# Optimization experiments

Hardware: AMD Instinct MI355X
Metric: run time of the kernel (lower is better)

Reference implementation:

```python
import jax, jax.numpy as jnp
import numpy as np

N, E, B = 100000, 800000, 64
IN, HC1, HC2, NC, SA = 256, 128, 32, 2, 350
NEG = 0.2  # GATv2Conv default negative_slope


def forward(s_x, s_edge_index, s_batch, s_root_n_id,
            Wq, bq, Wk, bk, Wv, bv,
            Wl1, bl1, Wr1, br1, att1, bias1,
            Wl2, bl2, Wr2, br2, att2, bias2,
            Wl3, bl3, Wr3, br3, att3, bias3,
            c1w, c1b, c2W, c2b, c3W, c3b,
            linW, linb, aW1, ab1, aW2, mW1, mb1, mW2, mb2):
    src, dst = s_edge_index[0], s_edge_index[1]
    x_info = s_x
    # --- SelfAttention over seq_len=1 (x.unsqueeze(1)) ---
    z = s_x[:, None, :]                                   # [N,1,IN]
    q = z @ Wq + bq; k = z @ Wk + bk; v = z @ Wv + bv      # [N,1,SA]
    scores = jnp.einsum('nqd,nkd->nqk', q, k) / jnp.sqrt(jnp.float32(SA))
    probs = jax.nn.softmax(scores, axis=-1)
    h = jnp.einsum('nqk,nkd->nqd', probs, v)[:, 0, :]      # [N,SA]

    def gatv2(x, Wl, bl, Wr, br, att, bias):
        # PyG GATv2Conv, heads=1, eval mode (dropout off)
        xl = x @ Wl + bl                                   # source transform [N,O]
        xr = x @ Wr + br                                   # target transform [N,O]
        e = jax.nn.leaky_relu(xl[src] + xr[dst], NEG)      # [E,O]
        s = e @ att                                        # [E]
        smax = jax.ops.segment_max(s, dst, num_segments=N)
        smax = jnp.where(jnp.isfinite(smax), smax, 0.0)
        ex = jnp.exp(s - smax[dst])
        den = jax.ops.segment_sum(ex, dst, num_segments=N)
        alpha = ex / jnp.maximum(den[dst], 1e-16)
        return jax.ops.segment_sum(alpha[:, None] * xl[src], dst, num_segments=N) + bias

    h = jax.nn.relu(gatv2(h, Wl1, bl1, Wr1, br1, att1, bias1))
    h = jax.nn.relu(gatv2(h, Wl2, bl2, Wr2, br2, att2, bias2))
    h = jax.nn.relu(gatv2(h, Wl3, bl3, Wr3, br3, att3, bias3))   # [N,HC2]

    # --- readout: root node feature ++ global mean pool ---
    cnt = jax.ops.segment_sum(jnp.ones((N,), h.dtype), s_batch, num_segments=B)
    pooled = jax.ops.segment_sum(h, s_batch, num_segments=B) / jnp.maximum(cnt, 1.0)[:, None]
    sx = jnp.concatenate([h[s_root_n_id], pooled], axis=-1)       # [B,2*HC2]

    # --- info branch on raw root features ---
    info = x_info[s_root_n_id]                                    # [B,IN]
    info = c1w[0] * info[:, :-2] + c1w[1] * info[:, 1:-1] + c1w[2] * info[:, 2:] + c1b  # Conv1d(1,1,3)
    t = info.T                                                    # [IN-2,B]
    t = jax.nn.relu(c2W @ t + c2b[:, None])                       # [HC1,B]
    t = jax.nn.relu(c3W @ t + c3b[:, None])                       # [HC1//2,B]
    t = t.T                                                       # [B,HC1//2]
    L = t.shape[1]
    t = jax.nn.relu(t.reshape(B, HC2, L // HC2).mean(-1))         # AdaptiveAvgPool1d(HC2)

    sx = jax.nn.relu(sx @ linW + linb)                            # [B,HC2]

    # --- semantic attention over the two views ---
    emb = jnp.stack([sx, t], axis=1)                              # [B,2,HC2]
    w = jnp.tanh(emb @ aW1 + ab1) @ aW2                           # [B,2,1]
    beta = jax.nn.softmax(w, axis=1)
    emb = (beta * emb).sum(1)                                     # [B,HC2]

    return jax.nn.softmax(jnp.tanh(emb @ mW1 + mb1) @ mW2 + mb2, axis=1)  # [B,NC]


def setup_inputs() -> dict:
    keys = iter(jax.random.split(jax.random.key(0), 64))
    def nrm(*shape):
        return jax.random.normal(next(keys), shape, dtype=jnp.float32) * 0.05
    inp = {}
    inp['s_x'] = jax.random.normal(next(keys), (N, IN), dtype=jnp.float32)
    inp['s_edge_index'] = jax.random.randint(next(keys), (2, E), 0, N)
    inp['s_batch'] = jnp.sort(jax.random.randint(next(keys), (N,), 0, B))
    inp['s_root_n_id'] = jax.random.randint(next(keys), (B,), 0, N)
    inp['Wq'] = nrm(IN, SA); inp['bq'] = nrm(SA)
    inp['Wk'] = nrm(IN, SA); inp['bk'] = nrm(SA)
    inp['Wv'] = nrm(IN, SA); inp['bv'] = nrm(SA)
    inp['Wl1'] = nrm(SA, HC1); inp['bl1'] = nrm(HC1)
    inp['Wr1'] = nrm(SA, HC1); inp['br1'] = nrm(HC1)
    inp['att1'] = nrm(HC1); inp['bias1'] = nrm(HC1)
    inp['Wl2'] = nrm(HC1, HC1 // 2); inp['bl2'] = nrm(HC1 // 2)
    inp['Wr2'] = nrm(HC1, HC1 // 2); inp['br2'] = nrm(HC1 // 2)
    inp['att2'] = nrm(HC1 // 2); inp['bias2'] = nrm(HC1 // 2)
    inp['Wl3'] = nrm(HC1 // 2, HC2); inp['bl3'] = nrm(HC2)
    inp['Wr3'] = nrm(HC1 // 2, HC2); inp['br3'] = nrm(HC2)
    inp['att3'] = nrm(HC2); inp['bias3'] = nrm(HC2)
    inp['c1w'] = nrm(3); inp['c1b'] = nrm(1)
    inp['c2W'] = nrm(HC1, IN - 2); inp['c2b'] = nrm(HC1)
    inp['c3W'] = nrm(HC1 // 2, HC1); inp['c3b'] = nrm(HC1 // 2)
    inp['linW'] = nrm(2 * HC2, HC2); inp['linb'] = nrm(HC2)
    inp['aW1'] = nrm(HC2, 16); inp['ab1'] = nrm(16); inp['aW2'] = nrm(16, 1)
    inp['mW1'] = nrm(HC2, 16); inp['mb1'] = nrm(16)
    inp['mW2'] = nrm(16, NC); inp['mb2'] = nrm(NC)
    return inp


def reference(s_x, s_edge_index, s_batch, s_root_n_id,
              Wq, bq, Wk, bk, Wv, bv,
              Wl1, bl1, Wr1, br1, att1, bias1,
              Wl2, bl2, Wr2, br2, att2, bias2,
              Wl3, bl3, Wr3, br3, att3, bias3,
              c1w, c1b, c2W, c2b, c3W, c3b,
              linW, linb, aW1, ab1, aW2, mW1, mb1, mW2, mb2):
    return forward(s_x, s_edge_index, s_batch, s_root_n_id,
                   Wq, bq, Wk, bk, Wv, bv,
                   Wl1, bl1, Wr1, br1, att1, bias1,
                   Wl2, bl2, Wr2, br2, att2, bias2,
                   Wl3, bl3, Wr3, br3, att3, bias3,
                   c1w, c1b, c2W, c2b, c3W, c3b,
                   linW, linb, aW1, ab1, aW2, mW1, mb1, mW2, mb2)
```

## Files before the change

kernel.cpp:

```cpp
#include <hip/hip_runtime.h>
#include <hip/hip_bf16.h>
#include <math.h>

typedef unsigned short ushort_t;
typedef __attribute__((ext_vector_type(8))) short bfrag;
typedef __attribute__((ext_vector_type(4))) float ffrag;

constexpr int N_NODES = 100000;
constexpr int N_EDGES = 800000;
constexpr int NB      = 64;
constexpr int IN_F    = 256;
constexpr int HC1C    = 128;
constexpr int HC2C    = 32;
constexpr int SA_D    = 350;
constexpr float NEG   = 0.2f;

constexpr int SCAN_NBLK = (N_NODES + 255) / 256;
constexpr int MB128     = (N_NODES + 127) / 128;

constexpr size_t OFF_WT1    = 0;
constexpr size_t OFF_WT2    = OFF_WT1 + 65536;
constexpr size_t OFF_WT3    = OFF_WT2 + 16384;
constexpr size_t OFF_BC1    = OFF_WT3 + 4096;
constexpr size_t OFF_BC2    = OFF_BC1 + 256;
constexpr size_t OFF_BC3    = OFF_BC2 + 128;
constexpr size_t OFF_XLR    = OFF_BC3 + 64;
constexpr size_t OFF_H      = OFF_XLR + (size_t)N_NODES * 256;
constexpr size_t OFF_DEG    = OFF_H + (size_t)N_NODES * 128;
constexpr size_t OFF_ROWPTR = OFF_DEG + N_NODES;
constexpr size_t OFF_CURSOR = OFF_ROWPTR + N_NODES + 1;
constexpr size_t OFF_BLKS   = OFF_CURSOR + N_NODES;
constexpr size_t OFF_BLKO   = OFF_BLKS + 512;
constexpr size_t OFF_CSRSRC = OFF_BLKO + 512;
constexpr size_t OFF_POOLED = OFF_CSRSRC + N_EDGES;
constexpr size_t OFF_CNT    = OFF_POOLED + NB * HC2C;
constexpr size_t OFF_SX     = OFF_CNT + NB;
constexpr size_t OFF_INFO   = OFF_SX + NB * HC2C;
constexpr size_t OFF_T1     = OFF_INFO + (size_t)NB * (IN_F - 2);
constexpr size_t OFF_T2     = OFF_T1 + (size_t)HC1C * NB;
constexpr size_t OFF_TT     = OFF_T2 + (size_t)NB * NB;
constexpr size_t WS_FLOATS  = OFF_TT + NB * HC2C;

__device__ __forceinline__ ushort_t f2bf(float f) {
  union { float f; unsigned int u; } a;
  a.f = f;
  unsigned int r = a.u + 0x7FFFu + ((a.u >> 16) & 1u);
  return (ushort_t)(r >> 16);
}
__device__ __forceinline__ float bf2f(ushort_t h) {
  union { unsigned int u; float f; } a;
  a.u = ((unsigned int)h) << 16;
  return a.f;
}
__device__ __forceinline__ float2 bfp(unsigned int u) {
  float2 r;
  r.x = __uint_as_float(u << 16);
  r.y = __uint_as_float(u & 0xFFFF0000u);
  return r;
}
__device__ __forceinline__ unsigned int pack2(float a, float b) {
  unsigned int ua = __float_as_uint(a);
  ua += 0x7FFFu + ((ua >> 16) & 1u);
  unsigned int ub = __float_as_uint(b);
  ub += 0x7FFFu + ((ub >> 16) & 1u);
  return __builtin_amdgcn_perm(ub, ua, 0x07060302u);
}

__global__ void k_wcomb(const float* __restrict__ Wv, const float* __restrict__ Wl1,
                        const float* __restrict__ Wr1, ushort_t* __restrict__ WT) {
  int t = blockIdx.x * blockDim.x + threadIdx.x;
  if (t >= 256 * 256) return;
  int n = t & 255;
  int k = t >> 8;
  const float* Wx = (n < 128) ? Wl1 : Wr1;
  int j = n & 127;
  float a = 0.f;
  for (int kk = 0; kk < SA_D; ++kk) a += Wv[k * SA_D + kk] * Wx[kk * 128 + j];
  WT[(size_t)n * 256 + k] = f2bf(a);
}

__global__ void k_bcomb(const float* __restrict__ bv, const float* __restrict__ Wl1,
                        const float* __restrict__ bl1, const float* __restrict__ Wr1,
                        const float* __restrict__ br1, float* __restrict__ bc) {
  int n = threadIdx.x;
  if (n >= 256) return;
  const float* Wx = (n < 128) ? Wl1 : Wr1;
  const float* bx = (n < 128) ? bl1 : br1;
  int j = n & 127;
  float a = bx[j];
  for (int kk = 0; kk < SA_D; ++kk) a += bv[kk] * Wx[kk * 128 + j];
  bc[n] = a;
}

template <int K, int C>
__global__ void k_wpack(const float* __restrict__ Wl, const float* __restrict__ bl,
                        const float* __restrict__ Wr, const float* __restrict__ br,
                        ushort_t* __restrict__ WT, float* __restrict__ bc) {
  constexpr int NN = 2 * C;
  int t = blockIdx.x * blockDim.x + threadIdx.x;
  if (t < NN) bc[t] = (t < C) ? bl[t] : br[t - C];
  if (t >= NN * K) return;
  int n = t % NN;
  int k = t / NN;
  float v = (n < C) ? Wl[k * C + n] : Wr[k * C + (n - C)];
  WT[(size_t)n * K + k] = f2bf(v);
}

__global__ void k_hist(const int* __restrict__ dst, int* __restrict__ deg) {
  int e = blockIdx.x * blockDim.x + threadIdx.x;
  if (e < N_EDGES) atomicAdd(deg + dst[e], 1);
}

__global__ void k_scan_local(const int* __restrict__ deg, int* __restrict__ row_ptr,
                             int* __restrict__ blk_sum) {
  __shared__ int sh[256];
  int t = threadIdx.x;
  int i = blockIdx.x * 256 + t;
  int v = (i < N_NODES) ? deg[i] : 0;
  sh[t] = v;
  __syncthreads();
  for (int off = 1; off < 256; off <<= 1) {
    int add = (t >= off) ? sh[t - off] : 0;
    __syncthreads();
    sh[t] += add;
    __syncthreads();
  }
  if (i < N_NODES) row_ptr[i] = sh[t] - v;
  if (t == 255) blk_sum[blockIdx.x] = sh[255];
}

__global__ void k_scan_blk(const int* __restrict__ blk_sum, int* __restrict__ blk_off) {
  __shared__ int sh[512];
  int t = threadIdx.x;
  int v = (t < SCAN_NBLK) ? blk_sum[t] : 0;
  sh[t] = v;
  __syncthreads();
  for (int off = 1; off < 512; off <<= 1) {
    int add = (t >= off) ? sh[t - off] : 0;
    __syncthreads();
    sh[t] += add;
    __syncthreads();
  }
  blk_off[t] = sh[t] - v;
}

__global__ void k_scan_add(int* __restrict__ row_ptr, const int* __restrict__ blk_off,
                           int* __restrict__ cursor) {
  int i = blockIdx.x * blockDim.x + threadIdx.x;
  if (i < N_NODES) {
    int v = row_ptr[i] + blk_off[i >> 8];
    row_ptr[i] = v;
    cursor[i] = v;
  }
  if (i == 0) row_ptr[N_NODES] = N_EDGES;
}

__global__ void k_fill(const int* __restrict__ src, const int* __restrict__ dst,
                       int* __restrict__ cursor, int* __restrict__ csr_src) {
  int e = blockIdx.x * blockDim.x + threadIdx.x;
  if (e >= N_EDGES) return;
  int pos = atomicAdd(cursor + dst[e], 1);
  csr_src[pos] = src[e];
}

template <int K, int NN, int BN, bool AF32>
__global__ __launch_bounds__(256) void k_gemm_bf16(const void* __restrict__ xin,
                                                   const ushort_t* __restrict__ WT,
                                                   const float* __restrict__ bc,
                                                   ushort_t* __restrict__ out, int M) {
  constexpr int BM    = 128;
  constexpr int BK    = 64;
  constexpr int LDA   = BK + 8;
  constexpr int RT    = 4;
  constexpr int CT    = BN / 32;
  constexpr int NSTEP = K / BK;
  __shared__ ushort_t As[BM * LDA];
  __shared__ ushort_t Bs[BN * LDA];
  const int tid  = threadIdx.x;
  const int wave = tid >> 6;
  const int wrow = wave >> 1;
  const int wcol = wave & 1;
  const int lane = tid & 63;
  const int quad = lane >> 4;
  const int l16  = lane & 15;
  const int m0   = blockIdx.x * BM;
  const int n0   = blockIdx.y * BN;

  const int arow = tid >> 1;
  const int aks  = (tid & 1) * 32;
  int gm = m0 + arow;
  if (gm >= M) gm = M - 1;

  ffrag acc[RT][CT];
#pragma unroll
  for (int rt = 0; rt < RT; ++rt)
#pragma unroll
    for (int ct = 0; ct < CT; ++ct) acc[rt][ct] = ffrag{0.f, 0.f, 0.f, 0.f};

  for (int i = 0; i < NSTEP; ++i) {
    const int k0 = i * BK;
    if (i) __syncthreads();
    if (AF32) {
      const float4* sp = (const float4*)((const float*)xin + (size_t)gm * K + k0 + aks);
      float4 f[8];
#pragma unroll
      for (int j = 0; j < 8; ++j) f[j] = sp[j];
      unsigned int d[16];
#pragma unroll
      for (int j = 0; j < 8; ++j) {
        d[2 * j]     = pack2(f[j].x, f[j].y);
        d[2 * j + 1] = pack2(f[j].z, f[j].w);
      }
#pragma unroll
      for (int j = 0; j < 4; ++j)
        *(uint4*)&As[arow * LDA + aks + j * 8] = *(uint4*)&d[j * 4];
    } else {
      const uint4* sp = (const uint4*)((const ushort_t*)xin + (size_t)gm * K + k0 + aks);
      uint4 u[4];
#pragma unroll
      for (int j = 0; j < 4; ++j) u[j] = sp[j];
#pragma unroll
      for (int j = 0; j < 4; ++j)
        *(uint4*)&As[arow * LDA + aks + j * 8] = u[j];
    }
#pragma unroll
    for (int c = 0; c < BN / 32; ++c) {
      int ch = tid + c * 256;
      int n  = ch >> 3;
      int ks = (ch & 7) * 8;
      *(uint4*)&Bs[n * LDA + ks] = *(const uint4*)(WT + (size_t)(n0 + n) * K + k0 + ks);
    }
    __syncthreads();
#pragma unroll
    for (int kh = 0; kh < 2; ++kh) {
      bfrag a[RT], b[CT];
#pragma unroll
      for (int rt = 0; rt < RT; ++rt)
        a[rt] = *(const bfrag*)&As[(wrow * 64 + rt * 16 + l16) * LDA + kh * 32 + quad * 8];
#pragma unroll
      for (int ct = 0; ct < CT; ++ct)
        b[ct] = *(const bfrag*)&Bs[(wcol * (BN / 2) + ct * 16 + l16) * LDA + kh * 32 + quad * 8];
#pragma unroll
      for (int ct = 0; ct < CT; ++ct)
#pragma unroll
        for (int rt = 0; rt < RT; ++rt)
          acc[rt][ct] = __builtin_amdgcn_mfma_f32_16x16x32_bf16(a[rt], b[ct], acc[rt][ct], 0, 0, 0);
    }
  }

#pragma unroll
  for (int rt = 0; rt < RT; ++rt)
#pragma unroll
    for (int ct = 0; ct < CT; ++ct) {
      int n = n0 + wcol * (BN / 2) + ct * 16 + l16;
      float b = bc[n];
#pragma unroll
      for (int r = 0; r < 4; ++r) {
        int m = m0 + wrow * 64 + rt * 16 + quad * 4 + r;
        if (m < M) out[(size_t)m * NN + n] = f2bf(acc[rt][ct][r] + b);
      }
    }
}

template <int C>
__global__ void k_gat(const ushort_t* __restrict__ xlr, const int* __restrict__ row_ptr,
                      const int* __restrict__ csr_src, const float* __restrict__ att,
                      const float* __restrict__ bias, ushort_t* __restrict__ h) {
  constexpr int G = C / 8;
  constexpr int RS = 2 * C;
  int t = blockIdx.x * blockDim.x + threadIdx.x;
  int d = t / G;
  int lane = t - d * G;
  if (d >= N_NODES) return;
  float xr[8], a[8];
  {
    uint4 u = *(const uint4*)(xlr + (size_t)d * RS + C + lane * 8);
    float2 p0 = bfp(u.x), p1 = bfp(u.y), p2 = bfp(u.z), p3 = bfp(u.w);
    xr[0] = p0.x; xr[1] = p0.y; xr[2] = p1.x; xr[3] = p1.y;
    xr[4] = p2.x; xr[5] = p2.y; xr[6] = p3.x; xr[7] = p3.y;
  }
  *(float4*)&a[0] = *(const float4*)(att + lane * 8);
  *(float4*)&a[4] = *(const float4*)(att + lane * 8 + 4);
  float acc[8];
#pragma unroll
  for (int j = 0; j < 8; ++j) acc[j] = 0.f;
  float den = 0.f;
  const int e0 = row_ptr[d], e1 = row_ptr[d + 1];
  int i = e0;
  for (; i + 2 <= e1; i += 2) {
    int s0 = csr_src[i];
    int s1 = csr_src[i + 1];
    uint4 u0 = *(const uint4*)(xlr + (size_t)s0 * RS + lane * 8);
    uint4 u1 = *(const uint4*)(xlr + (size_t)s1 * RS + lane * 8);
    float xl0[8], xl1[8];
    {
      float2 q0 = bfp(u0.x), q1 = bfp(u0.y), q2 = bfp(u0.z), q3 = bfp(u0.w);
      xl0[0] = q0.x; xl0[1] = q0.y; xl0[2] = q1.x; xl0[3] = q1.y;
      xl0[4] = q2.x; xl0[5] = q2.y; xl0[6] = q3.x; xl0[7] = q3.y;
      float2 r0 = bfp(u1.x), r1 = bfp(u1.y), r2 = bfp(u1.z), r3 = bfp(u1.w);
      xl1[0] = r0.x; xl1[1] = r0.y; xl1[2] = r1.x; xl1[3] = r1.y;
      xl1[4] = r2.x; xl1[5] = r2.y; xl1[6] = r3.x; xl1[7] = r3.y;
    }
    float p0 = 0.f, p1 = 0.f;
#pragma unroll
    for (int j = 0; j < 8; ++j) {
      float v0 = xl0[j] + xr[j];
      v0 = v0 > 0.f ? v0 : NEG * v0;
      p0 += a[j] * v0;
      float v1 = xl1[j] + xr[j];
      v1 = v1 > 0.f ? v1 : NEG * v1;
      p1 += a[j] * v1;
    }
#pragma unroll
    for (int off = G / 2; off > 0; off >>= 1) {
      p0 += __shfl_xor(p0, off, 64);
      p1 += __shfl_xor(p1, off, 64);
    }
    float ex0 = expf(p0);
    float ex1 = expf(p1);
    den += ex0 + ex1;
#pragma unroll
    for (int j = 0; j < 8; ++j) acc[j] += ex0 * xl0[j] + ex1 * xl1[j];
  }
  if (i < e1) {
    int s = csr_src[i];
    uint4 u = *(const uint4*)(xlr + (size_t)s * RS + lane * 8);
    float xl[8];
    {
      float2 q0 = bfp(u.x), q1 = bfp(u.y), q2 = bfp(u.z), q3 = bfp(u.w);
      xl[0] = q0.x; xl[1] = q0.y; xl[2] = q1.x; xl[3] = q1.y;
      xl[4] = q2.x; xl[5] = q2.y; xl[6] = q3.x; xl[7] = q3.y;
    }
    float p = 0.f;
#pragma unroll
    for (int j = 0; j < 8; ++j) {
      float v = xl[j] + xr[j];
      v = v > 0.f ? v : NEG * v;
      p += a[j] * v;
    }
#pragma unroll
    for (int off = G / 2; off > 0; off >>= 1) p += __shfl_xor(p, off, 64);
    float ex = expf(p);
    den += ex;
#pragma unroll
    for (int j = 0; j < 8; ++j) acc[j] += ex * xl[j];
  }
  float inv = 1.f / fmaxf(den, 1e-16f);
  float o[8];
#pragma unroll
  for (int j = 0; j < 8; ++j)
    o[j] = fmaxf(acc[j] * inv + bias[lane * 8 + j], 0.f);
  uint4 pk;
  pk.x = pack2(o[0], o[1]);
  pk.y = pack2(o[2], o[3]);
  pk.z = pack2(o[4], o[5]);
  pk.w = pack2(o[6], o[7]);
  *(uint4*)(h + (size_t)d * C + lane * 8) = pk;
}

__global__ void k_pool(const ushort_t* __restrict__ h3, const int* __restrict__ batch,
                       float* __restrict__ pooled, float* __restrict__ cnt) {
  constexpr int NPB = 1024;
  constexpr int NPT = NPB / 8;
  int c = threadIdx.x & 31;
  int r = threadIdx.x >> 5;
  int base = blockIdx.x * NPB + r * NPT;
  if (base >= N_NODES) return;
  int end = base + NPT;
  if (end > N_NODES) end = N_NODES;
  int cur_b = batch[base];
  float acc = 0.f, count = 0.f;
  for (int n = base; n < end; ++n) {
    int b = batch[n];
    if (b != cur_b) {
      atomicAdd(pooled + cur_b * HC2C + c, acc);
      if (c == 0) atomicAdd(cnt + cur_b, count);
      cur_b = b;
      acc = 0.f;
      count = 0.f;
    }
    acc += bf2f(h3[(size_t)n * HC2C + c]);
    count += 1.f;
  }
  atomicAdd(pooled + cur_b * HC2C + c, acc);
  if (c == 0) atomicAdd(cnt + cur_b, count);
}

__global__ void k_sx(const ushort_t* __restrict__ h3, const int* __restrict__ root,
                     const float* __restrict__ pooled, const float* __restrict__ cnt,
                     const float* __restrict__ linW, const float* __restrict__ linb,
                     float* __restrict__ sx) {
  int t = blockIdx.x * blockDim.x + threadIdx.x;
  if (t >= NB * HC2C) return;
  int b = t >> 5, j = t & 31;
  int r = root[b];
  float inv = 1.f / fmaxf(cnt[b], 1.0f);
  float a = linb[j];
  for (int c = 0; c < HC2C; ++c) a += bf2f(h3[(size_t)r * HC2C + c]) * linW[c * HC2C + j];
  for (int c = 0; c < HC2C; ++c) a += (pooled[b * HC2C + c] * inv) * linW[(HC2C + c) * HC2C + j];
  sx[t] = a > 0.f ? a : 0.f;
}

__global__ void k_info1(const float* __restrict__ X, const int* __restrict__ root,
                        const float* __restrict__ c1w, const float* __restrict__ c1b,
                        float* __restrict__ info) {
  constexpr int L = IN_F - 2;
  int t = blockIdx.x * blockDim.x + threadIdx.x;
  if (t >= NB * L) return;
  int b = t / L, i = t - (t / L) * L;
  const float* xr = X + (size_t)root[b] * IN_F;
  info[t] = c1w[0] * xr[i] + c1w[1] * xr[i + 1] + c1w[2] * xr[i + 2] + c1b[0];
}

__global__ void k_info2(const float* __restrict__ info, const float* __restrict__ c2W,
                        const float* __restrict__ c2b, float* __restrict__ t1) {
  constexpr int L = IN_F - 2;
  int t = blockIdx.x * blockDim.x + threadIdx.x;
  if (t >= HC1C * NB) return;
  int j = t >> 6, b = t & 63;
  float a = c2b[j];
  for (int i = 0; i < L; ++i) a += c2W[j * L + i] * info[b * L + i];
  t1[t] = a > 0.f ? a : 0.f;
}

__global__ void k_info3(const float* __restrict__ t1, const float* __restrict__ c3W,
                        const float* __restrict__ c3b, float* __restrict__ t2) {
  int t = blockIdx.x * blockDim.x + threadIdx.x;
  if (t >= NB * NB) return;
  int j = t >> 6, b = t & 63;
  float a = c3b[j];
  for (int i = 0; i < HC1C; ++i) a += c3W[j * HC1C + i] * t1[i * NB + b];
  t2[t] = a > 0.f ? a : 0.f;
}

__global__ void k_info4(const float* __restrict__ t2, float* __restrict__ tt) {
  int t = blockIdx.x * blockDim.x + threadIdx.x;
  if (t >= NB * HC2C) return;
  int b = t >> 5, c = t & 31;
  float v = 0.5f * (t2[(2 * c) * NB + b] + t2[(2 * c + 1) * NB + b]);
  tt[b * HC2C + c] = v > 0.f ? v : 0.f;
}

__global__ void k_final(const float* __restrict__ sx, const float* __restrict__ tt,
                        const float* __restrict__ aW1, const float* __restrict__ ab1,
                        const float* __restrict__ aW2, const float* __restrict__ mW1,
                        const float* __restrict__ mb1, const float* __restrict__ mW2,
                        const float* __restrict__ mb2, float* __restrict__ out) {
  int b = threadIdx.x;
  if (b >= NB) return;
  const float* e0 = sx + b * HC2C;
  const float* e1 = tt + b * HC2C;
  float w[2];
#pragma unroll
  for (int r = 0; r < 2; ++r) {
    const float* eb = (r == 0) ? e0 : e1;
    float acc = 0.f;
    for (int j = 0; j < 16; ++j) {
      float z = ab1[j];
      for (int c = 0; c < HC2C; ++c) z += eb[c] * aW1[c * 16 + j];
      acc += tanhf(z) * aW2[j];
    }
    w[r] = acc;
  }
  float mx = fmaxf(w[0], w[1]);
  float x0 = expf(w[0] - mx), x1 = expf(w[1] - mx);
  float inv = 1.f / (x0 + x1);
  float b0 = x0 * inv, b1 = x1 * inv;
  float t16[16];
  for (int j = 0; j < 16; ++j) {
    float z = mb1[j];
    for (int c = 0; c < HC2C; ++c) z += (b0 * e0[c] + b1 * e1[c]) * mW1[c * 16 + j];
    t16[j] = tanhf(z);
  }
  float l0 = mb2[0], l1 = mb2[1];
  for (int j = 0; j < 16; ++j) {
    l0 += t16[j] * mW2[j * 2 + 0];
    l1 += t16[j] * mW2[j * 2 + 1];
  }
  float m2 = fmaxf(l0, l1);
  float y0 = expf(l0 - m2), y1 = expf(l1 - m2);
  float is = 1.f / (y0 + y1);
  out[b * 2 + 0] = y0 * is;
  out[b * 2 + 1] = y1 * is;
}

extern "C" void kernel_launch(void* const* d_in, const int* in_sizes, int n_in, void* d_out,
                              int out_size, void* d_ws, size_t ws_size, hipStream_t stream) {
  if (ws_size < WS_FLOATS * sizeof(float)) return;

  const float* s_x   = (const float*)d_in[0];
  const int*   edge  = (const int*)d_in[1];
  const int*   batch = (const int*)d_in[2];
  const int*   root  = (const int*)d_in[3];
  const float* Wv    = (const float*)d_in[8];
  const float* bv    = (const float*)d_in[9];
  const float* Wl1   = (const float*)d_in[10];
  const float* bl1   = (const float*)d_in[11];
  const float* Wr1   = (const float*)d_in[12];
  const float* br1   = (const float*)d_in[13];
  const float* att1  = (const float*)d_in[14];
  const float* bias1 = (const float*)d_in[15];
  const float* Wl2   = (const float*)d_in[16];
  const float* bl2   = (const float*)d_in[17];
  const float* Wr2   = (const float*)d_in[18];
  const float* br2   = (const float*)d_in[19];
  const float* att2  = (const float*)d_in[20];
  const float* bias2 = (const float*)d_in[21];
  const float* Wl3   = (const float*)d_in[22];
  const float* bl3   = (const float*)d_in[23];
  const float* Wr3   = (const float*)d_in[24];
  const float* br3   = (const float*)d_in[25];
  const float* att3  = (const float*)d_in[26];
  const float* bias3 = (const float*)d_in[27];
  const float* c1w   = (const float*)d_in[28];
  const float* c1b   = (const float*)d_in[29];
  const float* c2W   = (const float*)d_in[30];
  const float* c2b   = (const float*)d_in[31];
  const float* c3W   = (const float*)d_in[32];
  const float* c3b   = (const float*)d_in[33];
  const float* linW  = (const float*)d_in[34];
  const float* linb  = (const float*)d_in[35];
  const float* aW1   = (const float*)d_in[36];
  const float* ab1   = (const float*)d_in[37];
  const float* aW2   = (const float*)d_in[38];
  const float* mW1   = (const float*)d_in[39];
  const float* mb1   = (const float*)d_in[40];
  const float* mW2   = (const float*)d_in[41];
  const float* mb2   = (const float*)d_in[42];

  const int* src = edge;
  const int* dst = edge + N_EDGES;

  float*    ws      = (float*)d_ws;
  ushort_t* WT1     = (ushort_t*)(ws + OFF_WT1);
  ushort_t* WT2     = (ushort_t*)(ws + OFF_WT2);
  ushort_t* WT3     = (ushort_t*)(ws + OFF_WT3);
  float*    bc1     = ws + OFF_BC1;
  float*    bc2     = ws + OFF_BC2;
  float*    bc3     = ws + OFF_BC3;
  ushort_t* xlr     = (ushort_t*)(ws + OFF_XLR);
  ushort_t* hbuf    = (ushort_t*)(ws + OFF_H);
  int*      deg     = (int*)(ws + OFF_DEG);
  int*      row_ptr = (int*)(ws + OFF_ROWPTR);
  int*      cursor  = (int*)(ws + OFF_CURSOR);
  int*      blks    = (int*)(ws + OFF_BLKS);
  int*      blko    = (int*)(ws + OFF_BLKO);
  int*      csr_src = (int*)(ws + OFF_CSRSRC);
  float*    pooled  = ws + OFF_POOLED;
  float*    cnt     = ws + OFF_CNT;
  float*    sx      = ws + OFF_SX;
  float*    info    = ws + OFF_INFO;
  float*    t1      = ws + OFF_T1;
  float*    t2      = ws + OFF_T2;
  float*    tt      = ws + OFF_TT;
  float*    out     = (float*)d_out;

  hipMemsetAsync(deg, 0, N_NODES * sizeof(int), stream);
  k_hist<<<(N_EDGES + 255) / 256, 256, 0, stream>>>(dst, deg);
  k_scan_local<<<SCAN_NBLK, 256, 0, stream>>>(deg, row_ptr, blks);
  k_scan_blk<<<1, 512, 0, stream>>>(blks, blko);
  k_scan_add<<<SCAN_NBLK, 256, 0, stream>>>(row_ptr, blko, cursor);
  k_fill<<<(N_EDGES + 255) / 256, 256, 0, stream>>>(src, dst, cursor, csr_src);

  k_wcomb<<<(256 * 256) / 256, 256, 0, stream>>>(Wv, Wl1, Wr1, WT1);
  k_bcomb<<<1, 256, 0, stream>>>(bv, Wl1, bl1, Wr1, br1, bc1);
  k_wpack<128, 64><<<(128 * 128 + 255) / 256, 256, 0, stream>>>(Wl2, bl2, Wr2, br2, WT2, bc2);
  k_wpack<64, 32><<<(64 * 64 + 255) / 256, 256, 0, stream>>>(Wl3, bl3, Wr3, br3, WT3, bc3);

  k_gemm_bf16<256, 256, 128, true><<<dim3(MB128, 2), 256, 0, stream>>>(s_x, WT1, bc1, xlr,
                                                                       N_NODES);
  k_gat<128><<<(N_NODES * 16 + 255) / 256, 256, 0, stream>>>(xlr, row_ptr, csr_src, att1,
                                                             bias1, hbuf);

  k_gemm_bf16<128, 128, 128, false><<<dim3(MB128, 1), 256, 0, stream>>>(hbuf, WT2, bc2, xlr,
                                                                        N_NODES);
  k_gat<64><<<(N_NODES * 8 + 255) / 256, 256, 0, stream>>>(xlr, row_ptr, csr_src, att2,
                                                           bias2, hbuf);

  k_gemm_bf16<64, 64, 64, false><<<dim3(MB128, 1), 256, 0, stream>>>(hbuf, WT3, bc3, xlr,
                                                                     N_NODES);
  k_gat<32><<<(N_NODES * 4 + 255) / 256, 256, 0, stream>>>(xlr, row_ptr, csr_src, att3,
                                                           bias3, hbuf);

  hipMemsetAsync(pooled, 0, (NB * HC2C + NB) * sizeof(float), stream);
  k_pool<<<(N_NODES + 1023) / 1024, 256, 0, stream>>>(hbuf, batch, pooled, cnt);
  k_sx<<<(NB * HC2C + 255) / 256, 256, 0, stream>>>(hbuf, root, pooled, cnt, linW, linb, sx);

  k_info1<<<(NB * (IN_F - 2) + 255) / 256, 256, 0, stream>>>(s_x, root, c1w, c1b, info);
  k_info2<<<(HC1C * NB + 255) / 256, 256, 0, stream>>>(info, c2W, c2b, t1);
  k_info3<<<(NB * NB + 255) / 256, 256, 0, stream>>>(t1, c3W, c3b, t2);
  k_info4<<<(NB * HC2C + 255) / 256, 256, 0, stream>>>(t2, tt);

  k_final<<<1, NB, 0, stream>>>(sx, tt, aW1, ab1, aW2, mW1, mb1, mW2, mb2, out);
}
```

Measured before the change: 655.1 us.

## Fuse weight-pack and tail kernels, shrink GEMM K-tile, unroll GAT edges by four

Merges the four weight-packing kernels into one launch and the six readout/info/final kernels into one per-graph block kernel that keeps intermediates in shared memory. The bf16 GEMM K-tile drops from 64 to 32, with one MFMA step per tile and a simpler B load. The GAT aggregation loop now handles four edges at a time to put more gathers in flight. The aim is fewer launches and more memory-level parallelism, at the cost of twice as many GEMM barriers and higher register pressure in the GAT loop.

```diff
diff --git a/kernel.cpp b/kernel.cpp
--- a/kernel.cpp
+++ b/kernel.cpp
@@ -34,12 +34,7 @@
 constexpr size_t OFF_CSRSRC = OFF_BLKO + 512;
 constexpr size_t OFF_POOLED = OFF_CSRSRC + N_EDGES;
 constexpr size_t OFF_CNT    = OFF_POOLED + NB * HC2C;
-constexpr size_t OFF_SX     = OFF_CNT + NB;
-constexpr size_t OFF_INFO   = OFF_SX + NB * HC2C;
-constexpr size_t OFF_T1     = OFF_INFO + (size_t)NB * (IN_F - 2);
-constexpr size_t OFF_T2     = OFF_T1 + (size_t)HC1C * NB;
-constexpr size_t OFF_TT     = OFF_T2 + (size_t)NB * NB;
-constexpr size_t WS_FLOATS  = OFF_TT + NB * HC2C;
+constexpr size_t WS_FLOATS  = OFF_CNT + NB;
 
 __device__ __forceinline__ ushort_t f2bf(float f) {
   union { float f; unsigned int u; } a;
@@ -65,45 +60,53 @@
   ub += 0x7FFFu + ((ub >> 16) & 1u);
   return __builtin_amdgcn_perm(ub, ua, 0x07060302u);
 }
-
-__global__ void k_wcomb(const float* __restrict__ Wv, const float* __restrict__ Wl1,
-                        const float* __restrict__ Wr1, ushort_t* __restrict__ WT) {
-  int t = blockIdx.x * blockDim.x + threadIdx.x;
-  if (t >= 256 * 256) return;
-  int n = t & 255;
-  int k = t >> 8;
-  const float* Wx = (n < 128) ? Wl1 : Wr1;
-  int j = n & 127;
-  float a = 0.f;
-  for (int kk = 0; kk < SA_D; ++kk) a += Wv[k * SA_D + kk] * Wx[kk * 128 + j];
-  WT[(size_t)n * 256 + k] = f2bf(a);
-}
-
-__global__ void k_bcomb(const float* __restrict__ bv, const float* __restrict__ Wl1,
-                        const float* __restrict__ bl1, const float* __restrict__ Wr1,
-                        const float* __restrict__ br1, float* __restrict__ bc) {
-  int n = threadIdx.x;
-  if (n >= 256) return;
-  const float* Wx = (n < 128) ? Wl1 : Wr1;
-  const float* bx = (n < 128) ? bl1 : br1;
-  int j = n & 127;
-  float a = bx[j];
-  for (int kk = 0; kk < SA_D; ++kk) a += bv[kk] * Wx[kk * 128 + j];
-  bc[n] = a;
-}
-
-template <int K, int C>
-__global__ void k_wpack(const float* __restrict__ Wl, const float* __restrict__ bl,
-                        const float* __restrict__ Wr, const float* __restrict__ br,
-                        ushort_t* __restrict__ WT, float* __restrict__ bc) {
-  constexpr int NN = 2 * C;
-  int t = blockIdx.x * blockDim.x + threadIdx.x;
-  if (t < NN) bc[t] = (t < C) ? bl[t] : br[t - C];
-  if (t >= NN * K) return;
-  int n = t % NN;
-  int k = t / NN;
-  float v = (n < C) ? Wl[k * C + n] : Wr[k * C + (n - C)];
-  WT[(size_t)n * K + k] = f2bf(v);
+__device__ __forceinline__ void unp8(uint4 u, float* x) {
+  float2 p0 = bfp(u.x), p1 = bfp(u.y), p2 = bfp(u.z), p3 = bfp(u.w);
+  x[0] = p0.x; x[1] = p0.y; x[2] = p1.x; x[3] = p1.y;
+  x[4] = p2.x; x[5] = p2.y; x[6] = p3.x; x[7] = p3.y;
+}
+
+__global__ void k_pack_all(const float* __restrict__ Wv, const float* __restrict__ bv,
+                           const float* __restrict__ Wl1, const float* __restrict__ bl1,
+                           const float* __restrict__ Wr1, const float* __restrict__ br1,
+                           const float* __restrict__ Wl2, const float* __restrict__ bl2,
+                           const float* __restrict__ Wr2, const float* __restrict__ br2,
+                           const float* __restrict__ Wl3, const float* __restrict__ bl3,
+                           const float* __restrict__ Wr3, const float* __restrict__ br3,
+                           ushort_t* __restrict__ WT1, float* __restrict__ bc1,
+                           ushort_t* __restrict__ WT2, float* __restrict__ bc2,
+                           ushort_t* __restrict__ WT3, float* __restrict__ bc3) {
+  int blk = blockIdx.x;
+  int tid = threadIdx.x;
+  if (blk < 256) {
+    int t = blk * 256 + tid;
+    int n = t & 255, k = t >> 8;
+    const float* Wx = (n < 128) ? Wl1 : Wr1;
+    int j = n & 127;
+    float a = 0.f;
+    for (int kk = 0; kk < SA_D; ++kk) a += Wv[k * SA_D + kk] * Wx[kk * 128 + j];
+    WT1[(size_t)n * 256 + k] = f2bf(a);
+  } else if (blk == 256) {
+    int n = tid;
+    const float* Wx = (n < 128) ? Wl1 : Wr1;
+    const float* bx = (n < 128) ? bl1 : br1;
+    int j = n & 127;
+    float a = bx[j];
+    for (int kk = 0; kk < SA_D; ++kk) a += bv[kk] * Wx[kk * 128 + j];
+    bc1[n] = a;
+  } else if (blk < 321) {
+    int t = (blk - 257) * 256 + tid;
+    int n = t & 127, k = t >> 7;
+    if (t < 128) bc2[t] = (t < 64) ? bl2[t] : br2[t - 64];
+    float v = (n < 64) ? Wl2[k * 64 + n] : Wr2[k * 64 + (n - 64)];
+    WT2[(size_t)n * 128 + k] = f2bf(v);
+  } else {
+    int t = (blk - 321) * 256 + tid;
+    int n = t & 63, k = t >> 6;
+    if (t < 64) bc3[t] = (t < 32) ? bl3[t] : br3[t - 32];
+    float v = (n < 32) ? Wl3[k * 32 + n] : Wr3[k * 32 + (n - 32)];
+    WT3[(size_t)n * 64 + k] = f2bf(v);
+  }
 }
 
 __global__ void k_hist(const int* __restrict__ dst, int* __restrict__ deg) {
@@ -169,7 +172,7 @@
                                                    const float* __restrict__ bc,
                                                    ushort_t* __restrict__ out, int M) {
   constexpr int BM    = 128;
-  constexpr int BK    = 64;
+  constexpr int BK    = 32;
   constexpr int LDA   = BK + 8;
   constexpr int RT    = 4;
   constexpr int CT    = BN / 32;
@@ -187,7 +190,7 @@
   const int n0   = blockIdx.y * BN;
 
   const int arow = tid >> 1;
-  const int aks  = (tid & 1) * 32;
+  const int aks  = (tid & 1) * 16;
   int gm = m0 + arow;
   if (gm >= M) gm = M - 1;
 
@@ -202,50 +205,47 @@
     if (i) __syncthreads();
     if (AF32) {
       const float4* sp = (const float4*)((const float*)xin + (size_t)gm * K + k0 + aks);
-      float4 f[8];
-#pragma unroll
-      for (int j = 0; j < 8; ++j) f[j] = sp[j];
-      unsigned int d[16];
-#pragma unroll
-      for (int j = 0; j < 8; ++j) {
+      float4 f[4];
+#pragma unroll
+      for (int j = 0; j < 4; ++j) f[j] = sp[j];
+      unsigned int d[8];
+#pragma unroll
+      for (int j = 0; j < 4; ++j) {
         d[2 * j]     = pack2(f[j].x, f[j].y);
         d[2 * j + 1] = pack2(f[j].z, f[j].w);
       }
-#pragma unroll
-      for (int j = 0; j < 4; ++j)
-        *(uint4*)&As[arow * LDA + aks + j * 8] = *(uint4*)&d[j * 4];
+      *(uint4*)&As[arow * LDA + aks]     = *(uint4*)&d[0];
+      *(uint4*)&As[arow * LDA + aks + 8] = *(uint4*)&d[4];
     } else {
       const uint4* sp = (const uint4*)((const ushort_t*)xin + (size_t)gm * K + k0 + aks);
-      uint4 u[4];
-#pragma unroll
-      for (int j = 0; j < 4; ++j) u[j] = sp[j];
-#pragma unroll
-      for (int j = 0; j < 4; ++j)
-        *(uint4*)&As[arow * LDA + aks + j * 8] = u[j];
-    }
-#pragma unroll
-    for (int c = 0; c < BN / 32; ++c) {
-      int ch = tid + c * 256;
-      int n  = ch >> 3;
-      int ks = (ch & 7) * 8;
-      *(uint4*)&Bs[n * LDA + ks] = *(const uint4*)(WT + (size_t)(n0 + n) * K + k0 + ks);
+      uint4 u0 = sp[0], u1 = sp[1];
+      *(uint4*)&As[arow * LDA + aks]     = u0;
+      *(uint4*)&As[arow * LDA + aks + 8] = u1;
+    }
+    if (BN == 128) {
+      int bn  = tid >> 1;
+      int bks = (tid & 1) * 16;
+      const ushort_t* gp = WT + (size_t)(n0 + bn) * K + k0 + bks;
+      *(uint4*)&Bs[bn * LDA + bks]     = *(const uint4*)gp;
+      *(uint4*)&Bs[bn * LDA + bks + 8] = *(const uint4*)(gp + 8);
+    } else {
+      int bn  = tid >> 2;
+      int bks = (tid & 3) * 8;
+      *(uint4*)&Bs[bn * LDA + bks] = *(const uint4*)(WT + (size_t)(n0 + bn) * K + k0 + bks);
     }
     __syncthreads();
-#pragma unroll
-    for (int kh = 0; kh < 2; ++kh) {
-      bfrag a[RT], b[CT];
+    bfrag a[RT], b[CT];
+#pragma unroll
+    for (int rt = 0; rt < RT; ++rt)
+      a[rt] = *(const bfrag*)&As[(wrow * 64 + rt * 16 + l16) * LDA + quad * 8];
+#pragma unroll
+    for (int ct = 0; ct < CT; ++ct)
+      b[ct] = *(const bfrag*)&Bs[(wcol * (BN / 2) + ct * 16 + l16) * LDA + quad * 8];
+#pragma unroll
+    for (int ct = 0; ct < CT; ++ct)
 #pragma unroll
       for (int rt = 0; rt < RT; ++rt)
-        a[rt] = *(const bfrag*)&As[(wrow * 64 + rt * 16 + l16) * LDA + kh * 32 + quad * 8];
-#pragma unroll
-      for (int ct = 0; ct < CT; ++ct)
-        b[ct] = *(const bfrag*)&Bs[(wcol * (BN / 2) + ct * 16 + l16) * LDA + kh * 32 + quad * 8];
-#pragma unroll
-      for (int ct = 0; ct < CT; ++ct)
-#pragma unroll
-        for (int rt = 0; rt < RT; ++rt)
-          acc[rt][ct] = __builtin_amdgcn_mfma_f32_16x16x32_bf16(a[rt], b[ct], acc[rt][ct], 0, 0, 0);
-    }
+        acc[rt][ct] = __builtin_amdgcn_mfma_f32_16x16x32_bf16(a[rt], b[ct], acc[rt][ct], 0, 0, 0);
   }
 
 #pragma unroll
@@ -273,12 +273,7 @@
   int lane = t - d * G;
   if (d >= N_NODES) return;
   float xr[8], a[8];
-  {
-    uint4 u = *(const uint4*)(xlr + (size_t)d * RS + C + lane * 8);
-    float2 p0 = bfp(u.x), p1 = bfp(u.y), p2 = bfp(u.z), p3 = bfp(u.w);
-    xr[0] = p0.x; xr[1] = p0.y; xr[2] = p1.x; xr[3] = p1.y;
-    xr[4] = p2.x; xr[5] = p2.y; xr[6] = p3.x; xr[7] = p3.y;
-  }
+  unp8(*(const uint4*)(xlr + (size_t)d * RS + C + lane * 8), xr);
   *(float4*)&a[0] = *(const float4*)(att + lane * 8);
   *(float4*)&a[4] = *(const float4*)(att + lane * 8 + 4);
   float acc[8];
@@ -287,50 +282,41 @@
   float den = 0.f;
   const int e0 = row_ptr[d], e1 = row_ptr[d + 1];
   int i = e0;
-  for (; i + 2 <= e1; i += 2) {
-    int s0 = csr_src[i];
-    int s1 = csr_src[i + 1];
-    uint4 u0 = *(const uint4*)(xlr + (size_t)s0 * RS + lane * 8);
-    uint4 u1 = *(const uint4*)(xlr + (size_t)s1 * RS + lane * 8);
-    float xl0[8], xl1[8];
-    {
-      float2 q0 = bfp(u0.x), q1 = bfp(u0.y), q2 = bfp(u0.z), q3 = bfp(u0.w);
-      xl0[0] = q0.x; xl0[1] = q0.y; xl0[2] = q1.x; xl0[3] = q1.y;
-      xl0[4] = q2.x; xl0[5] = q2.y; xl0[6] = q3.x; xl0[7] = q3.y;
-      float2 r0 = bfp(u1.x), r1 = bfp(u1.y), r2 = bfp(u1.z), r3 = bfp(u1.w);
-      xl1[0] = r0.x; xl1[1] = r0.y; xl1[2] = r1.x; xl1[3] = r1.y;
-      xl1[4] = r2.x; xl1[5] = r2.y; xl1[6] = r3.x; xl1[7] = r3.y;
-    }
-    float p0 = 0.f, p1 = 0.f;
+  for (; i + 4 <= e1; i += 4) {
+    uint4 u[4];
+#pragma unroll
+    for (int q = 0; q < 4; ++q)
+      u[q] = *(const uint4*)(xlr + (size_t)csr_src[i + q] * RS + lane * 8);
+    float xl[4][8];
+#pragma unroll
+    for (int q = 0; q < 4; ++q) unp8(u[q], xl[q]);
+    float p[4] = {0.f, 0.f, 0.f, 0.f};
 #pragma unroll
     for (int j = 0; j < 8; ++j) {
-      float v0 = xl0[j] + xr[j];
-      v0 = v0 > 0.f ? v0 : NEG * v0;
-      p0 += a[j] * v0;
-      float v1 = xl1[j] + xr[j];
-      v1 = v1 > 0.f ? v1 : NEG * v1;
-      p1 += a[j] * v1;
+#pragma unroll
+      for (int q = 0; q < 4; ++q) {
+        float v = xl[q][j] + xr[j];
+        v = v > 0.f ? v : NEG * v;
+        p[q] += a[j] * v;
+      }
     }
 #pragma unroll
     for (int off = G / 2; off > 0; off >>= 1) {
-      p0 += __shfl_xor(p0, off, 64);
-      p1 += __shfl_xor(p1, off, 64);
-    }
-    float ex0 = expf(p0);
-    float ex1 = expf(p1);
-    den += ex0 + ex1;
-#pragma unroll
-    for (int j = 0; j < 8; ++j) acc[j] += ex0 * xl0[j] + ex1 * xl1[j];
-  }
-  if (i < e1) {
+#pragma unroll
+      for (int q = 0; q < 4; ++q) p[q] += __shfl_xor(p[q], off, 64);
+    }
+    float ex[4];
+#pragma unroll
+    for (int q = 0; q < 4; ++q) ex[q] = expf(p[q]);
+    den += (ex[0] + ex[1]) + (ex[2] + ex[3]);
+#pragma unroll
+    for (int j = 0; j < 8; ++j)
+      acc[j] += (ex[0] * xl[0][j] + ex[1] * xl[1][j]) + (ex[2] * xl[2][j] + ex[3] * xl[3][j]);
+  }
+  for (; i < e1; ++i) {
     int s = csr_src[i];
-    uint4 u = *(const uint4*)(xlr + (size_t)s * RS + lane * 8);
     float xl[8];
-    {
-      float2 q0 = bfp(u.x), q1 = bfp(u.y), q2 = bfp(u.z), q3 = bfp(u.w);
-      xl[0] = q0.x; xl[1] = q0.y; xl[2] = q1.x; xl[3] = q1.y;
-      xl[4] = q2.x; xl[5] = q2.y; xl[6] = q3.x; xl[7] = q3.y;
-    }
+    unp8(*(const uint4*)(xlr + (size_t)s * RS + lane * 8), xl);
     float p = 0.f;
 #pragma unroll
     for (int j = 0; j < 8; ++j) {
@@ -386,102 +372,84 @@
   if (c == 0) atomicAdd(cnt + cur_b, count);
 }
 
-__global__ void k_sx(const ushort_t* __restrict__ h3, const int* __restrict__ root,
-                     const float* __restrict__ pooled, const float* __restrict__ cnt,
-                     const float* __restrict__ linW, const float* __restrict__ linb,
-                     float* __restrict__ sx) {
-  int t = blockIdx.x * blockDim.x + threadIdx.x;
-  if (t >= NB * HC2C) return;
-  int b = t >> 5, j = t & 31;
-  int r = root[b];
-  float inv = 1.f / fmaxf(cnt[b], 1.0f);
-  float a = linb[j];
-  for (int c = 0; c < HC2C; ++c) a += bf2f(h3[(size_t)r * HC2C + c]) * linW[c * HC2C + j];
-  for (int c = 0; c < HC2C; ++c) a += (pooled[b * HC2C + c] * inv) * linW[(HC2C + c) * HC2C + j];
-  sx[t] = a > 0.f ? a : 0.f;
-}
-
-__global__ void k_info1(const float* __restrict__ X, const int* __restrict__ root,
-                        const float* __restrict__ c1w, const float* __restrict__ c1b,
-                        float* __restrict__ info) {
+__global__ __launch_bounds__(256) void k_tail(
+    const ushort_t* __restrict__ h3, const int* __restrict__ root,
+    const float* __restrict__ pooled, const float* __restrict__ cnt,
+    const float* __restrict__ linW, const float* __restrict__ linb,
+    const float* __restrict__ X, const float* __restrict__ c1w,
+    const float* __restrict__ c1b, const float* __restrict__ c2W,
+    const float* __restrict__ c2b, const float* __restrict__ c3W,
+    const float* __restrict__ c3b, const float* __restrict__ aW1,
+    const float* __restrict__ ab1, const float* __restrict__ aW2,
+    const float* __restrict__ mW1, const float* __restrict__ mb1,
+    const float* __restrict__ mW2, const float* __restrict__ mb2,
+    float* __restrict__ out) {
   constexpr int L = IN_F - 2;
-  int t = blockIdx.x * blockDim.x + threadIdx.x;
-  if (t >= NB * L) return;
-  int b = t / L, i = t - (t / L) * L;
-  const float* xr = X + (size_t)root[b] * IN_F;
-  info[t] = c1w[0] * xr[i] + c1w[1] * xr[i + 1] + c1w[2] * xr[i + 2] + c1b[0];
-}
-
-__global__ void k_info2(const float* __restrict__ info, const float* __restrict__ c2W,
-                        const float* __restrict__ c2b, float* __restrict__ t1) {
-  constexpr int L = IN_F - 2;
-  int t = blockIdx.x * blockDim.x + threadIdx.x;
-  if (t >= HC1C * NB) return;
-  int j = t >> 6, b = t & 63;
-  float a = c2b[j];
-  for (int i = 0; i < L; ++i) a += c2W[j * L + i] * info[b * L + i];
-  t1[t] = a > 0.f ? a : 0.f;
-}
-
-__global__ void k_info3(const float* __restrict__ t1, const float* __restrict__ c3W,
-                        const float* __restrict__ c3b, float* __restrict__ t2) {
-  int t = blockIdx.x * blockDim.x + threadIdx.x;
-  if (t >= NB * NB) return;
-  int j = t >> 6, b = t & 63;
-  float a = c3b[j];
-  for (int i = 0; i < HC1C; ++i) a += c3W[j * HC1C + i] * t1[i * NB + b];
-  t2[t] = a > 0.f ? a : 0.f;
-}
-
-__global__ void k_info4(const float* __restrict__ t2, float* __restrict__ tt) {
-  int t = blockIdx.x * blockDim.x + threadIdx.x;
-  if (t >= NB * HC2C) return;
-  int b = t >> 5, c = t & 31;
-  float v = 0.5f * (t2[(2 * c) * NB + b] + t2[(2 * c + 1) * NB + b]);
-  tt[b * HC2C + c] = v > 0.f ? v : 0.f;
-}
-
-__global__ void k_final(const float* __restrict__ sx, const float* __restrict__ tt,
-                        const float* __restrict__ aW1, const float* __restrict__ ab1,
-                        const float* __restrict__ aW2, const float* __restrict__ mW1,
-                        const float* __restrict__ mb1, const float* __restrict__ mW2,
-                        const float* __restrict__ mb2, float* __restrict__ out) {
-  int b = threadIdx.x;
-  if (b >= NB) return;
-  const float* e0 = sx + b * HC2C;
-  const float* e1 = tt + b * HC2C;
-  float w[2];
-#pragma unroll
-  for (int r = 0; r < 2; ++r) {
-    const float* eb = (r == 0) ? e0 : e1;
-    float acc = 0.f;
+  __shared__ float s_info[L];
+  __shared__ float s_t1[HC1C];
+  __shared__ float s_t2[HC1C / 2];
+  __shared__ float s_e0[HC2C];
+  __shared__ float s_e1[HC2C];
+  const int b = blockIdx.x;
+  const int tid = threadIdx.x;
+  const int r = root[b];
+  const float* xr = X + (size_t)r * IN_F;
+  for (int i = tid; i < L; i += 256)
+    s_info[i] = c1w[0] * xr[i] + c1w[1] * xr[i + 1] + c1w[2] * xr[i + 2] + c1b[0];
+  __syncthreads();
+  if (tid < HC1C) {
+    float a = c2b[tid];
+    for (int i = 0; i < L; ++i) a += c2W[tid * L + i] * s_info[i];
+    s_t1[tid] = fmaxf(a, 0.f);
+  }
+  __syncthreads();
+  if (tid < HC1C / 2) {
+    float a = c3b[tid];
+    for (int i = 0; i < HC1C; ++i) a += c3W[tid * HC1C + i] * s_t1[i];
+    s_t2[tid] = fmaxf(a, 0.f);
+  }
+  __syncthreads();
+  if (tid < HC2C) {
+    float v = 0.5f * (s_t2[2 * tid] + s_t2[2 * tid + 1]);
+    s_e1[tid] = fmaxf(v, 0.f);
+  } else if (tid < 2 * HC2C) {
+    int j = tid - HC2C;
+    float inv = 1.f / fmaxf(cnt[b], 1.f);
+    float a = linb[j];
+    for (int c = 0; c < HC2C; ++c) a += bf2f(h3[(size_t)r * HC2C + c]) * linW[c * HC2C + j];
+    for (int c = 0; c < HC2C; ++c) a += pooled[b * HC2C + c] * inv * linW[(HC2C + c) * HC2C + j];
+    s_e0[j] = fmaxf(a, 0.f);
+  }
+  __syncthreads();
+  if (tid == 0) {
+    float w0 = 0.f, w1 = 0.f;
     for (int j = 0; j < 16; ++j) {
-      float z = ab1[j];
-      for (int c = 0; c < HC2C; ++c) z += eb[c] * aW1[c * 16 + j];
-      acc += tanhf(z) * aW2[j];
-    }
-    w[r] = acc;
-  }
-  float mx = fmaxf(w[0], w[1]);
-  float x0 = expf(w[0] - mx), x1 = expf(w[1] - mx);
-  float inv = 1.f / (x0 + x1);
-  float b0 = x0 * inv, b1 = x1 * inv;
-  float t16[16];
-  for (int j = 0; j < 16; ++j) {
-    float z = mb1[j];
-    for (int c = 0; c < HC2C; ++c) z += (b0 * e0[c] + b1 * e1[c]) * mW1[c * 16 + j];
-    t16[j] = tanhf(z);
-  }
-  float l0 = mb2[0], l1 = mb2[1];
-  for (int j = 0; j < 16; ++j) {
-    l0 += t16[j] * mW2[j * 2 + 0];
-    l1 += t16[j] * mW2[j * 2 + 1];
-  }
-  float m2 = fmaxf(l0, l1);
-  float y0 = expf(l0 - m2), y1 = expf(l1 - m2);
-  float is = 1.f / (y0 + y1);
-  out[b * 2 + 0] = y0 * is;
-  out[b * 2 + 1] = y1 * is;
+      float z0 = ab1[j], z1 = ab1[j];
+      for (int c = 0; c < HC2C; ++c) {
+        z0 += s_e0[c] * aW1[c * 16 + j];
+        z1 += s_e1[c] * aW1[c * 16 + j];
+      }
+      w0 += tanhf(z0) * aW2[j];
+      w1 += tanhf(z1) * aW2[j];
+    }
+    float mx = fmaxf(w0, w1);
+    float x0 = expf(w0 - mx), x1 = expf(w1 - mx);
+    float inv = 1.f / (x0 + x1);
+    float b0 = x0 * inv, b1 = x1 * inv;
+    float l0 = mb2[0], l1 = mb2[1];
+    for (int j = 0; j < 16; ++j) {
+      float z = mb1[j];
+      for (int c = 0; c < HC2C; ++c) z += (b0 * s_e0[c] + b1 * s_e1[c]) * mW1[c * 16 + j];
+      float tz = tanhf(z);
+      l0 += tz * mW2[j * 2 + 0];
+      l1 += tz * mW2[j * 2 + 1];
+    }
+    float m2 = fmaxf(l0, l1);
+    float y0 = expf(l0 - m2), y1 = expf(l1 - m2);
+    float is = 1.f / (y0 + y1);
+    out[b * 2 + 0] = y0 * is;
+    out[b * 2 + 1] = y1 * is;
+  }
 }
 
 extern "C" void kernel_launch(void* const* d_in, const int* in_sizes, int n_in, void* d_out,
@@ -548,11 +516,6 @@
   int*      csr_src = (int*)(ws + OFF_CSRSRC);
   float*    pooled  = ws + OFF_POOLED;
   float*    cnt     = ws + OFF_CNT;
-  float*    sx      = ws + OFF_SX;
-  float*    info    = ws + OFF_INFO;
-  float*    t1      = ws + OFF_T1;
-  float*    t2      = ws + OFF_T2;
-  float*    tt      = ws + OFF_TT;
   float*    out     = (float*)d_out;
 
   hipMemsetAsync(deg, 0, N_NODES * sizeof(int), stream);
@@ -562,10 +525,8 @@
   k_scan_add<<<SCAN_NBLK, 256, 0, stream>>>(row_ptr, blko, cursor);
   k_fill<<<(N_EDGES + 255) / 256, 256, 0, stream>>>(src, dst, cursor, csr_src);
 
-  k_wcomb<<<(256 * 256) / 256, 256, 0, stream>>>(Wv, Wl1, Wr1, WT1);
-  k_bcomb<<<1, 256, 0, stream>>>(bv, Wl1, bl1, Wr1, br1, bc1);
-  k_wpack<128, 64><<<(128 * 128 + 255) / 256, 256, 0, stream>>>(Wl2, bl2, Wr2, br2, WT2, bc2);
-  k_wpack<64, 32><<<(64 * 64 + 255) / 256, 256, 0, stream>>>(Wl3, bl3, Wr3, br3, WT3, bc3);
+  k_pack_all<<<337, 256, 0, stream>>>(Wv, bv, Wl1, bl1, Wr1, br1, Wl2, bl2, Wr2, br2, Wl3,
+                                      bl3, Wr3, br3, WT1, bc1, WT2, bc2, WT3, bc3);
 
   k_gemm_bf16<256, 256, 128, true><<<dim3(MB128, 2), 256, 0, stream>>>(s_x, WT1, bc1, xlr,
                                                                        N_NODES);
@@ -584,12 +545,6 @@
 
   hipMemsetAsync(pooled, 0, (NB * HC2C + NB) * sizeof(float), stream);
   k_pool<<<(N_NODES + 1023) / 1024, 256, 0, stream>>>(hbuf, batch, pooled, cnt);
-  k_sx<<<(NB * HC2C + 255) / 256, 256, 0, stream>>>(hbuf, root, pooled, cnt, linW, linb, sx);
-
-  k_info1<<<(NB * (IN_F - 2) + 255) / 256, 256, 0, stream>>>(s_x, root, c1w, c1b, info);
-  k_info2<<<(HC1C * NB + 255) / 256, 256, 0, stream>>>(info, c2W, c2b, t1);
-  k_info3<<<(NB * NB + 255) / 256, 256, 0, stream>>>(t1, c3W, c3b, t2);
-  k_info4<<<(NB * HC2C + 255) / 256, 256, 0, stream>>>(t2, tt);
-
-  k_final<<<1, NB, 0, stream>>>(sx, tt, aW1, ab1, aW2, mW1, mb1, mW2, mb2, out);
-}
+  k_tail<<<NB, 256, 0, stream>>>(hbuf, root, pooled, cnt, linW, linb, s_x, c1w, c1b, c2W,
+                                 c2b, c3W, c3b, aW1, ab1, aW2, mW1, mb1, mW2, mb2, out);
+}
```

Measured after the change: 638.8 us. 2.5% less time.
